# Optimization experiments

Measured on AMD Instinct MI355X. Metric: run time of the kernel, lower is better.

Reference implementation:

```python
import jax, jax.numpy as jnp
import numpy as np

TAU = 0.5

def setup_inputs() -> dict:
    key = jax.random.key(0)
    kx, ky = jax.random.split(key)
    B, H = 8192, 256
    x = jax.random.normal(kx, (B, H), dtype=jnp.float32)
    y = jax.random.normal(ky, (B, H), dtype=jnp.float32)
    return {"x": x, "y": y}

def reference(x, y):
    # L2-normalize rows
    x_norm = x / jnp.linalg.norm(x, axis=1, keepdims=True)
    y_norm = y / jnp.linalg.norm(y, axis=1, keepdims=True)
    xy_norm = jnp.concatenate([x_norm, y_norm], axis=0)  # [2N, H]
    yx_norm = jnp.concatenate([y_norm, x_norm], axis=0)  # [2N, H]
    # [2N, 2N] cosine-similarity matrix (dominant memory traffic)
    sim_mat_1 = xy_norm @ xy_norm.T
    exp_mat = jnp.exp(sim_mat_1 / TAU)
    exp_row_sum = jnp.sum(exp_mat, axis=1)
    exp_diag = jnp.diagonal(exp_mat)
    denominator = exp_row_sum - exp_diag
    # diag(xy_norm @ yx_norm.T) is the row-wise dot product (avoids redundant NxN matmul)
    pos_sim = jnp.sum(xy_norm * yx_norm, axis=1)
    numerator = jnp.exp(pos_sim / TAU)
    nt_xent = -jnp.log(numerator / denominator)
    return jnp.mean(nt_xent)
```

## Files before the change

### kernel.cpp

```cpp
#include <hip/hip_runtime.h>
#include <hip/hip_bf16.h>
#include <math.h>

constexpr int NROWS = 8192;
constexpr int HDIM  = 256;
constexpr int N2    = 16384;
constexpr int BM    = 128;
constexpr int BK    = 32;
constexpr int NCHUNK = HDIM / BK;
constexpr int NTILE = N2 / BM;
constexpr int NBLK  = NTILE * (NTILE + 1) / 2;

constexpr float PRESCALE = 1.69864357f;

typedef __attribute__((ext_vector_type(4))) float floatx4;
typedef __attribute__((ext_vector_type(8))) short shortx8;

__device__ __forceinline__ void async_copy16(const void* gptr, void* lptr) {
    __builtin_amdgcn_global_load_lds(
        (const __attribute__((address_space(1))) unsigned int*)gptr,
        (__attribute__((address_space(3))) unsigned int*)lptr, 16, 0, 0);
}

#define WAIT_VM4()   __builtin_amdgcn_s_waitcnt(0x0F74)
#define WAIT_VM0()   __builtin_amdgcn_s_waitcnt(0x0F70)
#define MEMFENCE()   __asm__ __volatile__("" ::: "memory")
#define RAW_BARRIER() do { MEMFENCE(); __builtin_amdgcn_s_barrier(); MEMFENCE(); } while (0)

#define DPP_ROW_SHL_ADD(v, CTRL) do {                                        \
    union { float f; int i; } _u, _r; _u.f = (v);                            \
    _r.i = __builtin_amdgcn_update_dpp(0, _u.i, (CTRL), 0xF, 0xF, true);     \
    (v) += _r.f; } while (0)

__global__ __launch_bounds__(256) void normalize_kernel(
    const float* __restrict__ x, const float* __restrict__ y,
    __hip_bfloat16* __restrict__ Z, float* __restrict__ pos,
    float* __restrict__ rowsum, float* __restrict__ out)
{
    const int wave = threadIdx.x >> 6, lane = threadIdx.x & 63;
    const int row  = blockIdx.x * 4 + wave;

    const float4 xv = ((const float4*)x)[row * 64 + lane];
    const float4 yv = ((const float4*)y)[row * 64 + lane];

    float sx  = xv.x*xv.x + xv.y*xv.y + xv.z*xv.z + xv.w*xv.w;
    float sy  = yv.x*yv.x + yv.y*yv.y + yv.z*yv.z + yv.w*yv.w;
    float sxy = xv.x*yv.x + xv.y*yv.y + xv.z*yv.z + xv.w*yv.w;
    #pragma unroll
    for (int m = 1; m < 64; m <<= 1) {
        sx  += __shfl_xor(sx,  m);
        sy  += __shfl_xor(sy,  m);
        sxy += __shfl_xor(sxy, m);
    }
    const float rxn = rsqrtf(sx), ryn = rsqrtf(sy);
    const float rx = rxn * PRESCALE, ry = ryn * PRESCALE;

    union { ushort4 u; __hip_bfloat16 h[4]; } zx, zy;
    zx.h[0] = __float2bfloat16(xv.x * rx); zx.h[1] = __float2bfloat16(xv.y * rx);
    zx.h[2] = __float2bfloat16(xv.z * rx); zx.h[3] = __float2bfloat16(xv.w * rx);
    zy.h[0] = __float2bfloat16(yv.x * ry); zy.h[1] = __float2bfloat16(yv.y * ry);
    zy.h[2] = __float2bfloat16(yv.z * ry); zy.h[3] = __float2bfloat16(yv.w * ry);
    ((ushort4*)Z)[row * 64 + lane]             = zx.u;
    ((ushort4*)Z)[(row + NROWS) * 64 + lane]   = zy.u;

    if (lane == 0) {
        const float p = sxy * rxn * ryn;
        pos[row]         = p;
        pos[row + NROWS] = p;
    }
    const int gt = blockIdx.x * 256 + threadIdx.x;
    if (gt < N2) rowsum[gt] = 0.f;
    if (gt == 0) out[0] = 0.f;
}

__global__ __launch_bounds__(256, 3) void simgemm_kernel(
    const __hip_bfloat16* __restrict__ Z, float* __restrict__ rowsum)
{
    const int b = blockIdx.x;
    const int k = b & 7;
    const int m = b >> 3;
    int bi, bj;
    if (m < 136) {
        int ti = (int)((33.0f - sqrtf(1089.0f - 8.0f * (float)m)) * 0.5f);
        if (m < ti * (33 - ti) / 2) ti--;
        else if (m >= (ti + 1) * (32 - ti) / 2) ti++;
        const int tj = ti + (m - ti * (33 - ti) / 2);
        bi = k * 16 + ti;
        bj = k * 16 + tj;
    } else {
        const int m2 = m - 136;
        const int hh = m2 >> 7;
        const int r  = m2 & 127;
        const int h  = hh * 8 + k;
        const int q  = h >> 1;
        const int sub = h & 1;
        int gi = 0;
        #pragma unroll
        for (int t = 6; t > 0; --t)
            if (q >= t * (15 - t) / 2) { gi = t; break; }
        const int gj = gi + 1 + (q - gi * (15 - gi) / 2);
        bi = gi * 16 + sub * 8 + (r >> 4);
        bj = gj * 16 + (r & 15);
    }
    const bool diag = (bi == bj);

    __shared__ alignas(16) __hip_bfloat16 tiles[6 * BM * BK];
    __shared__ float rs[BM];
    __shared__ float cs[BM];
    __hip_bfloat16* tA = tiles;
    __hip_bfloat16* tB = tiles + BM * BK;

    const int tid  = threadIdx.x;
    const int wave = tid >> 6;
    const int lane = tid & 63;
    const int wm   = wave & 1;
    const int wn   = wave >> 1;
    const int g    = lane >> 4;
    const int m15  = lane & 15;

    if (tid < BM) { rs[tid] = 0.f; cs[tid] = 0.f; }

    const int st_r0  = wave * 32 + (lane >> 2);
    const int st_c   = (lane & 3) ^ ((lane >> 3) & 3);
    const __hip_bfloat16* gA0 = Z + (size_t)(bi * BM + st_r0) * HDIM + st_c * 8;
    const __hip_bfloat16* gA1 = gA0 + 16 * HDIM;
    const __hip_bfloat16* gB0 = Z + (size_t)(bj * BM + st_r0) * HDIM + st_c * 8;
    const __hip_bfloat16* gB1 = gB0 + 16 * HDIM;
    __hip_bfloat16* lA0 = tA + (wave * 32) * BK;
    __hip_bfloat16* lA1 = tA + (wave * 32 + 16) * BK;
    __hip_bfloat16* lB0 = tB + (wave * 32) * BK;
    __hip_bfloat16* lB1 = tB + (wave * 32 + 16) * BK;

    const int sw = g ^ ((m15 >> 1) & 3);
    const __hip_bfloat16* rA = tA + (wm * 64 + m15) * BK + sw * 8;
    const __hip_bfloat16* rB = tB + (wn * 64 + m15) * BK + sw * 8;

    floatx4 acc[4][4] = {};

    #define STAGE(ck)  do {                                                  \
        const int _o = ((ck) % 3) * 2 * BM * BK;                             \
        async_copy16(gA0 + (ck) * BK, lA0 + _o);                             \
        async_copy16(gA1 + (ck) * BK, lA1 + _o);                             \
        async_copy16(gB0 + (ck) * BK, lB0 + _o);                             \
        async_copy16(gB1 + (ck) * BK, lB1 + _o);                             \
    } while (0)

    STAGE(0);

    #pragma unroll
    for (int s = 0; s < NCHUNK; ++s) {
        if (s + 1 < NCHUNK) { STAGE(s + 1); WAIT_VM4(); }
        else                { WAIT_VM0(); }
        RAW_BARRIER();

        const int bo = (s % 3) * 2 * BM * BK;
        shortx8 af[4], bfr[4];
        #pragma unroll
        for (int f = 0; f < 4; ++f) {
            af[f]  = *(const shortx8*)(rA + bo + f * 16 * BK);
            bfr[f] = *(const shortx8*)(rB + bo + f * 16 * BK);
        }
        #pragma unroll
        for (int fm = 0; fm < 4; ++fm)
            #pragma unroll
            for (int fn = 0; fn < 4; ++fn)
                acc[fm][fn] = __builtin_amdgcn_mfma_f32_16x16x32_bf16(
                    af[fm], bfr[fn], acc[fm][fn], 0, 0, 0);
    }
    #undef STAGE

    float rp[4][4] = {{0.f}};
    float cp[4]    = {0.f};

    if (!diag) {
        #pragma unroll
        for (int fm = 0; fm < 4; ++fm)
            #pragma unroll
            for (int fn = 0; fn < 4; ++fn) {
                const floatx4 a = acc[fm][fn];
                #pragma unroll
                for (int q = 0; q < 4; ++q) {
                    const float e = __builtin_amdgcn_exp2f(a[q]);
                    rp[fm][q] += e;
                    cp[fn]    += e;
                }
            }
    } else {
        #pragma unroll
        for (int fm = 0; fm < 4; ++fm)
            #pragma unroll
            for (int fn = 0; fn < 4; ++fn) {
                const floatx4 a = acc[fm][fn];
                const int cl = wn * 64 + fn * 16 + m15;
                #pragma unroll
                for (int q = 0; q < 4; ++q) {
                    const int rl = wm * 64 + fm * 16 + g * 4 + q;
                    float e = __builtin_amdgcn_exp2f(a[q]);
                    if (cl <= rl) e = 0.f;
                    rp[fm][q] += e;
                    cp[fn]    += e;
                }
            }
    }

    #pragma unroll
    for (int fm = 0; fm < 4; ++fm)
        #pragma unroll
        for (int q = 0; q < 4; ++q) {
            float v = rp[fm][q];
            DPP_ROW_SHL_ADD(v, 0x101);
            DPP_ROW_SHL_ADD(v, 0x102);
            DPP_ROW_SHL_ADD(v, 0x104);
            DPP_ROW_SHL_ADD(v, 0x108);
            rp[fm][q] = v;
        }
    if (m15 == 0) {
        #pragma unroll
        for (int fm = 0; fm < 4; ++fm)
            #pragma unroll
            for (int q = 0; q < 4; ++q)
                atomicAdd(&rs[wm * 64 + fm * 16 + g * 4 + q], rp[fm][q]);
    }

    #pragma unroll
    for (int mask = 16; mask < 64; mask <<= 1)
        #pragma unroll
        for (int fn = 0; fn < 4; ++fn)
            cp[fn] += __shfl_xor(cp[fn], mask);
    if (g == 0) {
        #pragma unroll
        for (int fn = 0; fn < 4; ++fn)
            atomicAdd(&cs[wn * 64 + fn * 16 + m15], cp[fn]);
    }

    __syncthreads();
    if (tid < BM) {
        atomicAdd(&rowsum[(size_t)bi * BM + tid], rs[tid]);
        atomicAdd(&rowsum[(size_t)bj * BM + tid], cs[tid]);
    }
}

__global__ __launch_bounds__(1024) void finalize_kernel(
    const float* __restrict__ rowsum, const float* __restrict__ pos,
    float* __restrict__ out)
{
    const int i = threadIdx.x + blockIdx.x * 1024;
    float s = logf(rowsum[i]) - 2.0f * pos[i];
    #pragma unroll
    for (int off = 32; off; off >>= 1) s += __shfl_down(s, off);
    __shared__ float sh[16];
    const int lt = threadIdx.x;
    if ((lt & 63) == 0) sh[lt >> 6] = s;
    __syncthreads();
    if (lt == 0) {
        float tot = 0.f;
        #pragma unroll
        for (int w = 0; w < 16; ++w) tot += sh[w];
        atomicAdd(out, tot / (float)N2);
    }
}

extern "C" void kernel_launch(void* const* d_in, const int* in_sizes, int n_in,
                              void* d_out, int out_size, void* d_ws, size_t ws_size,
                              hipStream_t stream)
{
    const float* x = (const float*)d_in[0];
    const float* y = (const float*)d_in[1];

    __hip_bfloat16* Z = (__hip_bfloat16*)d_ws;
    float* rowsum = (float*)((char*)d_ws + (size_t)N2 * HDIM * sizeof(__hip_bfloat16));
    float* pos    = rowsum + N2;

    normalize_kernel<<<NROWS / 4, 256, 0, stream>>>(x, y, Z, pos, rowsum, (float*)d_out);
    simgemm_kernel<<<NBLK, 256, 0, stream>>>(Z, rowsum);
    finalize_kernel<<<N2 / 1024, 1024, 0, stream>>>(rowsum, pos, (float*)d_out);
}
```

Measured before the change: 159.1 us.

## Enlarge similarity GEMM tiles to 256x256 with 512-thread blocks and MFMA priority

Doubles the output tile of the fused similarity/exp/rowsum kernel from 128x128 to 256x256. Blocks grow to 8 waves, each wave now owns a 128x64 sub-tile, and the triangular block-index mapping is rewritten for the coarser tiling. Larger tiles reuse each staged LDS operand across more MFMAs and halve the number of tile pairs and rowsum atomics. The MFMA loop is also wrapped in s_setprio to favour matrix issue. In exchange the accumulator register count doubles and the triple-buffered LDS footprint grows, which likely lowers the number of blocks resident per CU and leaves fewer blocks in total for load balancing.

New measurement: 155.6 us. 2.2% less time.

```diff
diff --git a/kernel.cpp b/kernel.cpp
--- a/kernel.cpp
+++ b/kernel.cpp
@@ -5,10 +5,10 @@
 constexpr int NROWS = 8192;
 constexpr int HDIM  = 256;
 constexpr int N2    = 16384;
-constexpr int BM    = 128;
+constexpr int TM    = 256;
 constexpr int BK    = 32;
 constexpr int NCHUNK = HDIM / BK;
-constexpr int NTILE = N2 / BM;
+constexpr int NTILE = N2 / TM;
 constexpr int NBLK  = NTILE * (NTILE + 1) / 2;
 
 constexpr float PRESCALE = 1.69864357f;
@@ -73,24 +73,24 @@
     if (gt == 0) out[0] = 0.f;
 }
 
-__global__ __launch_bounds__(256, 3) void simgemm_kernel(
+__global__ __launch_bounds__(512, 2) void simgemm_kernel(
     const __hip_bfloat16* __restrict__ Z, float* __restrict__ rowsum)
 {
     const int b = blockIdx.x;
     const int k = b & 7;
     const int m = b >> 3;
     int bi, bj;
-    if (m < 136) {
-        int ti = (int)((33.0f - sqrtf(1089.0f - 8.0f * (float)m)) * 0.5f);
-        if (m < ti * (33 - ti) / 2) ti--;
-        else if (m >= (ti + 1) * (32 - ti) / 2) ti++;
-        const int tj = ti + (m - ti * (33 - ti) / 2);
-        bi = k * 16 + ti;
-        bj = k * 16 + tj;
+    if (m < 36) {
+        int ti = (int)((17.0f - sqrtf(289.0f - 8.0f * (float)m)) * 0.5f);
+        if (m < ti * (17 - ti) / 2) ti--;
+        else if (m >= (ti + 1) * (16 - ti) / 2) ti++;
+        const int tj = ti + (m - ti * (17 - ti) / 2);
+        bi = k * 8 + ti;
+        bj = k * 8 + tj;
     } else {
-        const int m2 = m - 136;
-        const int hh = m2 >> 7;
-        const int r  = m2 & 127;
+        const int m2 = m - 36;
+        const int hh = m2 >> 5;
+        const int r  = m2 & 31;
         const int h  = hh * 8 + k;
         const int q  = h >> 1;
         const int sub = h & 1;
@@ -99,16 +99,16 @@
         for (int t = 6; t > 0; --t)
             if (q >= t * (15 - t) / 2) { gi = t; break; }
         const int gj = gi + 1 + (q - gi * (15 - gi) / 2);
-        bi = gi * 16 + sub * 8 + (r >> 4);
-        bj = gj * 16 + (r & 15);
+        bi = gi * 8 + sub * 4 + (r >> 3);
+        bj = gj * 8 + (r & 7);
     }
     const bool diag = (bi == bj);
 
-    __shared__ alignas(16) __hip_bfloat16 tiles[6 * BM * BK];
-    __shared__ float rs[BM];
-    __shared__ float cs[BM];
+    __shared__ alignas(16) __hip_bfloat16 tiles[6 * TM * BK];
+    __shared__ float rs[TM];
+    __shared__ float cs[TM];
     __hip_bfloat16* tA = tiles;
-    __hip_bfloat16* tB = tiles + BM * BK;
+    __hip_bfloat16* tB = tiles + TM * BK;
 
     const int tid  = threadIdx.x;
     const int wave = tid >> 6;
@@ -118,13 +118,13 @@
     const int g    = lane >> 4;
     const int m15  = lane & 15;
 
-    if (tid < BM) { rs[tid] = 0.f; cs[tid] = 0.f; }
+    if (tid < TM) { rs[tid] = 0.f; cs[tid] = 0.f; }
 
     const int st_r0  = wave * 32 + (lane >> 2);
     const int st_c   = (lane & 3) ^ ((lane >> 3) & 3);
-    const __hip_bfloat16* gA0 = Z + (size_t)(bi * BM + st_r0) * HDIM + st_c * 8;
+    const __hip_bfloat16* gA0 = Z + (size_t)(bi * TM + st_r0) * HDIM + st_c * 8;
     const __hip_bfloat16* gA1 = gA0 + 16 * HDIM;
-    const __hip_bfloat16* gB0 = Z + (size_t)(bj * BM + st_r0) * HDIM + st_c * 8;
+    const __hip_bfloat16* gB0 = Z + (size_t)(bj * TM + st_r0) * HDIM + st_c * 8;
     const __hip_bfloat16* gB1 = gB0 + 16 * HDIM;
     __hip_bfloat16* lA0 = tA + (wave * 32) * BK;
     __hip_bfloat16* lA1 = tA + (wave * 32 + 16) * BK;
@@ -132,13 +132,13 @@
     __hip_bfloat16* lB1 = tB + (wave * 32 + 16) * BK;
 
     const int sw = g ^ ((m15 >> 1) & 3);
-    const __hip_bfloat16* rA = tA + (wm * 64 + m15) * BK + sw * 8;
-    const __hip_bfloat16* rB = tB + (wn * 64 + m15) * BK + sw * 8;
-
-    floatx4 acc[4][4] = {};
+    const __hip_bfloat16* rA = tA + (wm * 128 + m15) * BK + sw * 8;
+    const __hip_bfloat16* rB = tB + (wn * 64  + m15) * BK + sw * 8;
+
+    floatx4 acc[8][4] = {};
 
     #define STAGE(ck)  do {                                                  \
-        const int _o = ((ck) % 3) * 2 * BM * BK;                             \
+        const int _o = ((ck) % 3) * 2 * TM * BK;                             \
         async_copy16(gA0 + (ck) * BK, lA0 + _o);                             \
         async_copy16(gA1 + (ck) * BK, lA1 + _o);                             \
         async_copy16(gB0 + (ck) * BK, lB0 + _o);                             \
@@ -153,28 +153,32 @@
         else                { WAIT_VM0(); }
         RAW_BARRIER();
 
-        const int bo = (s % 3) * 2 * BM * BK;
-        shortx8 af[4], bfr[4];
-        #pragma unroll
-        for (int f = 0; f < 4; ++f) {
+        const int bo = (s % 3) * 2 * TM * BK;
+        shortx8 af[8], bfr[4];
+        #pragma unroll
+        for (int f = 0; f < 8; ++f)
             af[f]  = *(const shortx8*)(rA + bo + f * 16 * BK);
+        #pragma unroll
+        for (int f = 0; f < 4; ++f)
             bfr[f] = *(const shortx8*)(rB + bo + f * 16 * BK);
-        }
-        #pragma unroll
-        for (int fm = 0; fm < 4; ++fm)
+
+        __builtin_amdgcn_s_setprio(1);
+        #pragma unroll
+        for (int fm = 0; fm < 8; ++fm)
             #pragma unroll
             for (int fn = 0; fn < 4; ++fn)
                 acc[fm][fn] = __builtin_amdgcn_mfma_f32_16x16x32_bf16(
                     af[fm], bfr[fn], acc[fm][fn], 0, 0, 0);
+        __builtin_amdgcn_s_setprio(0);
     }
     #undef STAGE
 
-    float rp[4][4] = {{0.f}};
+    float rp[8][4] = {{0.f}};
     float cp[4]    = {0.f};
 
     if (!diag) {
         #pragma unroll
-        for (int fm = 0; fm < 4; ++fm)
+        for (int fm = 0; fm < 8; ++fm)
             #pragma unroll
             for (int fn = 0; fn < 4; ++fn) {
                 const floatx4 a = acc[fm][fn];
@@ -187,14 +191,14 @@
             }
     } else {
         #pragma unroll
-        for (int fm = 0; fm < 4; ++fm)
+        for (int fm = 0; fm < 8; ++fm)
             #pragma unroll
             for (int fn = 0; fn < 4; ++fn) {
                 const floatx4 a = acc[fm][fn];
                 const int cl = wn * 64 + fn * 16 + m15;
                 #pragma unroll
                 for (int q = 0; q < 4; ++q) {
-                    const int rl = wm * 64 + fm * 16 + g * 4 + q;
+                    const int rl = wm * 128 + fm * 16 + g * 4 + q;
                     float e = __builtin_amdgcn_exp2f(a[q]);
                     if (cl <= rl) e = 0.f;
                     rp[fm][q] += e;
@@ -204,7 +208,7 @@
     }
 
     #pragma unroll
-    for (int fm = 0; fm < 4; ++fm)
+    for (int fm = 0; fm < 8; ++fm)
         #pragma unroll
         for (int q = 0; q < 4; ++q) {
             float v = rp[fm][q];
@@ -216,10 +220,10 @@
         }
     if (m15 == 0) {
         #pragma unroll
-        for (int fm = 0; fm < 4; ++fm)
+        for (int fm = 0; fm < 8; ++fm)
             #pragma unroll
             for (int q = 0; q < 4; ++q)
-                atomicAdd(&rs[wm * 64 + fm * 16 + g * 4 + q], rp[fm][q]);
+                atomicAdd(&rs[wm * 128 + fm * 16 + g * 4 + q], rp[fm][q]);
     }
 
     #pragma unroll
@@ -234,9 +238,9 @@
     }
 
     __syncthreads();
-    if (tid < BM) {
-        atomicAdd(&rowsum[(size_t)bi * BM + tid], rs[tid]);
-        atomicAdd(&rowsum[(size_t)bj * BM + tid], cs[tid]);
+    if (tid < TM) {
+        atomicAdd(&rowsum[(size_t)bi * TM + tid], rs[tid]);
+        atomicAdd(&rowsum[(size_t)bj * TM + tid], cs[tid]);
     }
 }
 
@@ -272,6 +276,6 @@
     float* pos    = rowsum + N2;
 
     normalize_kernel<<<NROWS / 4, 256, 0, stream>>>(x, y, Z, pos, rowsum, (float*)d_out);
-    simgemm_kernel<<<NBLK, 256, 0, stream>>>(Z, rowsum);
+    simgemm_kernel<<<NBLK, 512, 0, stream>>>(Z, rowsum);
     finalize_kernel<<<N2 / 1024, 1024, 0, stream>>>(rowsum, pos, (float*)d_out);
 }
```
